# Performance work log

Hardware: AMD Instinct MI355X
Metric: run time of the kernel (lower is better)

The kernel has to match this reference:

```python
import jax, jax.numpy as jnp
import numpy as np

N_NODES = 50000
N_EDGES = 1200000
N_REL = 40
N_BASES = 30
EMB = 64
HID = 128
N_GRAPHS = 64


def rgcn_layer(h, src, dst, edge_type, comp, basis, root, bias):
    # W_r = sum_b comp[r,b] * basis[b]  -> [R, in, out]
    W = jnp.einsum('rb,bio->rio', comp, basis)
    n = h.shape[0]
    # aggregate source features per (target node, relation): mean aggregation (PyG RGCNConv default)
    seg = dst * N_REL + edge_type                      # [E]
    msgs = h[src]                                      # [E, in]  (gather)
    agg = jax.ops.segment_sum(msgs, seg, num_segments=n * N_REL)
    agg = agg.reshape(n, N_REL, -1)                    # [N, R, in]
    cnt = jax.ops.segment_sum(jnp.ones((src.shape[0],), h.dtype), seg,
                              num_segments=n * N_REL).reshape(n, N_REL, 1)
    agg = agg / jnp.maximum(cnt, 1.0)
    out = jnp.einsum('nri,rio->no', agg, W) + h @ root + bias
    return out


def setup_inputs() -> dict:
    key = jax.random.key(0)
    ks = jax.random.split(key, 12)
    x = jnp.arange(N_NODES, dtype=jnp.int64) if jax.config.jax_enable_x64 else jnp.arange(N_NODES, dtype=jnp.int32)
    edge_index = jax.random.randint(ks[0], (2, N_EDGES), 0, N_NODES)
    edge_type = jax.random.randint(ks[1], (N_EDGES,), 0, N_REL)
    batch = jnp.sort(jax.random.randint(ks[2], (N_NODES,), 0, N_GRAPHS))
    s = 0.05
    node_emb = jax.random.normal(ks[3], (N_NODES, EMB), jnp.float32)
    comp1 = jax.random.normal(ks[4], (N_REL, N_BASES), jnp.float32) * s
    basis1 = jax.random.normal(ks[5], (N_BASES, EMB, HID), jnp.float32) * s
    root1 = jax.random.normal(ks[6], (EMB, HID), jnp.float32) * s
    bias1 = jnp.zeros((HID,), jnp.float32)
    comp2 = jax.random.normal(ks[7], (N_REL, N_BASES), jnp.float32) * s
    basis2 = jax.random.normal(ks[8], (N_BASES, HID, HID), jnp.float32) * s
    root2 = jax.random.normal(ks[9], (HID, HID), jnp.float32) * s
    bias2 = jnp.zeros((HID,), jnp.float32)
    return {"x": x, "edge_index": edge_index, "edge_type": edge_type, "batch": batch,
            "node_emb": node_emb,
            "comp1": comp1, "basis1": basis1, "root1": root1, "bias1": bias1,
            "comp2": comp2, "basis2": basis2, "root2": root2, "bias2": bias2}


def reference(x, edge_index, edge_type, batch, node_emb,
              comp1, basis1, root1, bias1, comp2, basis2, root2, bias2):
    src, dst = edge_index[0], edge_index[1]
    h = node_emb[x]                                              # embedding lookup
    h = jax.nn.relu(rgcn_layer(h, src, dst, edge_type, comp1, basis1, root1, bias1))
    h = jax.nn.relu(rgcn_layer(h, src, dst, edge_type, comp2, basis2, root2, bias2))
    # global mean pool over graphs in batch
    sums = jax.ops.segment_sum(h, batch, num_segments=N_GRAPHS)  # [G, HID]
    cnts = jax.ops.segment_sum(jnp.ones((h.shape[0],), h.dtype), batch,
                               num_segments=N_GRAPHS)[:, None]
    return sums / jnp.maximum(cnts, 1.0)
```

## Files before the change

kernel.cpp:

```cpp
#include <hip/hip_runtime.h>


#define N_NODES 50000
#define N_EDGES 1200000
#define N_REL   40
#define N_BASES 30
#define EMB     64
#define HID     128
#define N_GRAPHS 64

#define NKEYC_MAX 160
#define PERM_CAP  ((size_t)N_EDGES + (size_t)NKEYC_MAX * 256)
#define SP_EPB    1024

typedef float f32x4  __attribute__((ext_vector_type(4)));
typedef short bf16x8 __attribute__((ext_vector_type(8)));

__device__ __forceinline__ unsigned short f2bf(float x) {
    unsigned int u = __float_as_uint(x);
    u = (u + 0x7FFFu + ((u >> 16) & 1u)) >> 16;
    return (unsigned short)u;
}
__device__ __forceinline__ float bflo(unsigned int u) { return __uint_as_float(u << 16); }
__device__ __forceinline__ float bfhi(unsigned int u) { return __uint_as_float(u & 0xffff0000u); }

#define OFF_WF1   ((size_t)0)
#define OFF_WF2   ((size_t)163840)
#define OFF_CNT   ((size_t)491520)
#define OFF_H1    ((size_t)2491520)
#define OFF_H2    ((size_t)8891520)
#define OFF_HB1   ((size_t)15291520)
#define OFF_HB2   ((size_t)16891520)
#define OFF_CNTG  ((size_t)20091520)
#define OFF_POOL  ((size_t)20091584)
#define OFF_PSRC  ((size_t)20099776)
#define OFF_POS   ((size_t)21340736)
#define OFF_PDST  ((size_t)22581696)
#define OFF_HCR   ((size_t)23822656)
#define OFF_CCR   ((size_t)23822816)
#define OFF_POCR  ((size_t)23822976)
#define OFF_HD    ((size_t)23823168)
#define OFF_CD    ((size_t)23873168)
#define OFF_POD   ((size_t)23923168)
#define OFF_RF1   ((size_t)23973184)
#define OFF_RF2   ((size_t)23977280)
#define OFF_PM    ((size_t)23985472)

template <int IN, int KT>
__global__ void k_Wfrag(const float* __restrict__ comp, const float* __restrict__ basis,
                        unsigned short* __restrict__ Wf) {
    const int FR = IN * HID;
    int idx = blockIdx.x * blockDim.x + threadIdx.x;
    if (idx >= N_REL * FR) return;
    int r = idx / FR, F = idx - r * FR;
    int j = F & 7, lane = (F >> 3) & 63, tt = F >> 9;
    int kt = tt % KT, ct = tt / KT;
    int k = kt * 32 + (lane >> 4) * 8 + j;
    int c = ct * 16 + (lane & 15);
    float s = 0.f;
#pragma unroll
    for (int b = 0; b < N_BASES; ++b)
        s += comp[r * N_BASES + b] * basis[((size_t)b * IN + k) * HID + c];
    Wf[idx] = f2bf(s);
}

template <int IN, int KT>
__global__ void k_rootfrag(const float* __restrict__ root, unsigned short* __restrict__ rf) {
    int idx = blockIdx.x * blockDim.x + threadIdx.x;
    if (idx >= IN * HID) return;
    int j = idx & 7, lane = (idx >> 3) & 63, tt = idx >> 9;
    int kt = tt % KT, ct = tt / KT;
    int k = kt * 32 + (lane >> 4) * 8 + j;
    int c = ct * 16 + (lane & 15);
    rf[idx] = f2bf(root[k * HID + c]);
}

__global__ void k_count(const int* __restrict__ dst, const int* __restrict__ etype,
                        float* __restrict__ cnt) {
    int e = blockIdx.x * blockDim.x + threadIdx.x;
    if (e >= N_EDGES) return;
    atomicAdd(&cnt[(size_t)dst[e] * N_REL + etype[e]], 1.0f);
}

__global__ void k_deg_inv(float* __restrict__ cnt, int* __restrict__ hist) {
    int n = blockIdx.x * blockDim.x + threadIdx.x;
    if (n >= N_NODES) return;
    float* row = cnt + (size_t)n * N_REL;
    float s = 0.f;
#pragma unroll 8
    for (int r = 0; r < N_REL; ++r) {
        float c = row[r];
        s += c;
        row[r] = 1.0f / fmaxf(c, 1.0f);
    }
    hist[n] = (int)(s + 0.5f);
}

__global__ void k_scan_d(const int* __restrict__ hist, int* __restrict__ po) {
    __shared__ int csum[256];
    int t = threadIdx.x;
    const int CH = (N_NODES + 255) / 256;
    int k0 = t * CH, k1 = min(k0 + CH, N_NODES);
    int s = 0;
    for (int k = k0; k < k1; ++k) s += hist[k];
    csum[t] = s;
    __syncthreads();
    if (t == 0) {
        int acc = 0;
        for (int i = 0; i < 256; ++i) { int v = csum[i]; csum[i] = acc; acc += v; }
        po[N_NODES] = acc;
    }
    __syncthreads();
    int base = csum[t];
    for (int k = k0; k < k1; ++k) { po[k] = base; base += hist[k]; }
}

__global__ void k_hist_cr(const int* __restrict__ dst, const int* __restrict__ etype,
                          int* __restrict__ hist, int chn, int nkeyc) {
    __shared__ int lh[NKEYC_MAX];
    int t = threadIdx.x;
    if (t < nkeyc) lh[t] = 0;
    __syncthreads();
    int e = blockIdx.x * blockDim.x + t;
    if (e < N_EDGES) atomicAdd(&lh[(dst[e] / chn) * N_REL + etype[e]], 1);
    __syncthreads();
    if (t < nkeyc && lh[t]) atomicAdd(&hist[t], lh[t]);
}

__global__ void k_scan_cr(const int* __restrict__ hist, int* __restrict__ po, int nkeyc) {
    if (threadIdx.x == 0) {
        int acc = 0;
        for (int k = 0; k < nkeyc; ++k) {
            po[k] = acc;
            acc += ((hist[k] + 255) >> 8) << 8;
        }
        po[nkeyc] = acc;
    }
}

__global__ void k_fill(int* __restrict__ ps_src, int* __restrict__ ps_os,
                       int* __restrict__ ps_dst, int dumprow) {
    for (size_t s = (size_t)blockIdx.x * blockDim.x + threadIdx.x; s < PERM_CAP;
         s += (size_t)gridDim.x * blockDim.x) {
        ps_src[s] = 0;
        ps_os[s] = dumprow;
        ps_dst[s] = 0;
    }
}

__global__ void k_scatter_s(const int* __restrict__ src, const int* __restrict__ dst,
                            const int* __restrict__ etype,
                            const int* __restrict__ po_cr, int* __restrict__ cur_cr,
                            const int* __restrict__ po_d, int* __restrict__ cur_d,
                            int* __restrict__ ps_src, int* __restrict__ ps_os,
                            int* __restrict__ ps_dst, int chn, int nkeyc) {
    __shared__ int lh[NKEYC_MAX], sbase[NKEYC_MAX];
    int t = threadIdx.x;
    if (t < nkeyc) lh[t] = 0;
    __syncthreads();
    int e0 = blockIdx.x * SP_EPB;
    int e_[4], key_[4];
#pragma unroll
    for (int i = 0; i < 4; ++i) {
        int e = e0 + t + i * 256;
        e_[i] = e;
        if (e < N_EDGES) {
            key_[i] = (dst[e] / chn) * N_REL + etype[e];
            atomicAdd(&lh[key_[i]], 1);
        }
    }
    __syncthreads();
    if (t < nkeyc) { if (lh[t]) sbase[t] = atomicAdd(&cur_cr[t], lh[t]); lh[t] = 0; }
    __syncthreads();
#pragma unroll
    for (int i = 0; i < 4; ++i) {
        if (e_[i] < N_EDGES) {
            int e = e_[i], key = key_[i];
            int d = dst[e];
            int p = atomicAdd(&lh[key], 1);
            int slot = po_cr[key] + sbase[key] + p;
            int os_g = po_d[d] + atomicAdd(&cur_d[d], 1);
            int os_l = os_g - po_d[(d / chn) * chn];
            ps_src[slot] = src[e];
            ps_os[slot] = os_l;
            ps_dst[slot] = d;
        }
    }
}

template <int IN, int KT>
__global__ __launch_bounds__(256, 4)
void k_rootgemm(const unsigned short* __restrict__ hb_in,
                const unsigned short* __restrict__ rf,
                const float* __restrict__ bias, float* __restrict__ h) {
    __shared__ unsigned short Wl[8 * KT * 64 * 8];
    {
        const f32x4* Wg = (const f32x4*)rf;
        f32x4* Wd = (f32x4*)Wl;
        for (int kk = threadIdx.x; kk < 8 * KT * 64; kk += 256) Wd[kk] = Wg[kk];
    }
    __syncthreads();

    int l = threadIdx.x & 63, wv = threadIdx.x >> 6;
    int lrow = l & 15, lk = l >> 4;
    int nbase = blockIdx.x * 64 + wv * 16;

    int nrow = min(nbase + lrow, N_NODES - 1);
    bf16x8 a[KT];
    const unsigned short* hrow = hb_in + (size_t)nrow * IN + lk * 8;
#pragma unroll
    for (int kt = 0; kt < KT; ++kt)
        a[kt] = *(const bf16x8*)(hrow + kt * 32);

    f32x4 acc[8];
#pragma unroll
    for (int ct = 0; ct < 8; ++ct) acc[ct] = (f32x4){0.f, 0.f, 0.f, 0.f};
#pragma unroll
    for (int ct = 0; ct < 8; ++ct) {
#pragma unroll
        for (int kt = 0; kt < KT; ++kt) {
            bf16x8 bb = *(const bf16x8*)(Wl + ((ct * KT + kt) * 64 + l) * 8);
            acc[ct] = __builtin_amdgcn_mfma_f32_16x16x32_bf16(a[kt], bb, acc[ct], 0, 0, 0);
        }
    }
#pragma unroll
    for (int q = 0; q < 4; ++q) {
        int n = nbase + lk * 4 + q;
        if (n < N_NODES) {
#pragma unroll
            for (int ct = 0; ct < 8; ++ct)
                h[(size_t)n * HID + ct * 16 + lrow] = acc[ct][q] + bias[ct * 16 + lrow];
        }
    }
}

template <int IN, int KT>
__global__ __launch_bounds__(256, 4)
void k_msg(const unsigned short* __restrict__ hb_in, const int* __restrict__ ps_src,
           const int* __restrict__ ps_os, const int* __restrict__ ps_dst,
           const float* __restrict__ invc,
           const int* __restrict__ po_cr,
           const unsigned short* __restrict__ Wf, unsigned int* __restrict__ pm) {
    __shared__ unsigned short Wl[8 * KT * 64 * 8];
    int slot0 = po_cr[0] + blockIdx.x * 256;
    if (slot0 >= po_cr[N_REL]) return;
    int r = 0;
    while (po_cr[r + 1] <= slot0) ++r;

    {
        const f32x4* Wg = (const f32x4*)(Wf + (size_t)r * (8 * KT * 64 * 8));
        f32x4* Wd = (f32x4*)Wl;
        for (int kk = threadIdx.x; kk < 8 * KT * 64; kk += 256) Wd[kk] = Wg[kk];
    }
    __syncthreads();

    int l = threadIdx.x & 63, wv = threadIdx.x >> 6;
    int lrow = l & 15, lk = l >> 4;

    for (int t = wv; t < 16; t += 4) {
        int slot = slot0 + t * 16 + lrow;
        int sv = ps_src[slot];
        int os = ps_os[slot];
        int d  = ps_dst[slot];
        float inv = invc[(size_t)d * N_REL + r];

        bf16x8 a[KT];
        const unsigned short* hrow = hb_in + (size_t)sv * IN + lk * 8;
#pragma unroll
        for (int kt = 0; kt < KT; ++kt)
            a[kt] = *(const bf16x8*)(hrow + kt * 32);

        f32x4 acc[8];
#pragma unroll
        for (int ct = 0; ct < 8; ++ct) acc[ct] = (f32x4){0.f, 0.f, 0.f, 0.f};
#pragma unroll
        for (int ct = 0; ct < 8; ++ct) {
#pragma unroll
            for (int kt = 0; kt < KT; ++kt) {
                bf16x8 bb = *(const bf16x8*)(Wl + ((ct * KT + kt) * 64 + l) * 8);
                acc[ct] = __builtin_amdgcn_mfma_f32_16x16x32_bf16(a[kt], bb, acc[ct], 0, 0, 0);
            }
        }
#pragma unroll
        for (int q = 0; q < 4; ++q) {
            int row = lk * 4 + q;
            int osq   = __shfl(os, row);
            float ivq = __shfl(inv, row);
            unsigned int* dp = pm + (size_t)osq * 64 + lrow;
#pragma unroll
            for (int cp = 0; cp < 4; ++cp) {
                unsigned int u = (unsigned int)f2bf(acc[2 * cp][q] * ivq)
                               | ((unsigned int)f2bf(acc[2 * cp + 1][q] * ivq) << 16);
                dp[cp * 16] = u;
            }
        }
    }
}

template <bool WRITE_HB>
__global__ __launch_bounds__(256, 8)
void k_reduce(const unsigned int* __restrict__ pm, const int* __restrict__ po_d,
              int n0chunk, int chn, float* __restrict__ h,
              unsigned short* __restrict__ hb_out) {
    int wv = threadIdx.x >> 6, p = threadIdx.x & 63;
    int n = n0chunk + blockIdx.x * 4 + wv;
    if (n >= n0chunk + chn) return;
    int pmbase = po_d[n0chunk];
    int b0 = po_d[n] - pmbase;
    int cn = po_d[n + 1] - pmbase - b0;
    float lo = 0.f, hi = 0.f;
    const unsigned int* rp = pm + (size_t)b0 * 64 + p;
    int k = 0;
    for (; k + 4 <= cn; k += 4) {
        unsigned int u0 = rp[0], u1 = rp[64], u2 = rp[128], u3 = rp[192];
        rp += 256;
        lo += bflo(u0) + bflo(u1) + bflo(u2) + bflo(u3);
        hi += bfhi(u0) + bfhi(u1) + bfhi(u2) + bfhi(u3);
    }
    for (; k < cn; ++k) {
        unsigned int u = rp[0];
        rp += 64;
        lo += bflo(u); hi += bfhi(u);
    }
    int cA = (p & 15) + 32 * (p >> 4);
    float* hp = h + (size_t)n * HID;
    float vA = fmaxf(hp[cA] + lo, 0.f);
    float vB = fmaxf(hp[cA + 16] + hi, 0.f);
    hp[cA] = vA;
    hp[cA + 16] = vB;
    if (WRITE_HB) {
        hb_out[(size_t)n * HID + cA] = f2bf(vA);
        hb_out[(size_t)n * HID + cA + 16] = f2bf(vB);
    }
}

__global__ void k_cvt_emb(const float* __restrict__ emb, const int* __restrict__ x,
                          unsigned short* __restrict__ hb) {
    int idx = blockIdx.x * blockDim.x + threadIdx.x;
    if (idx >= N_NODES * (EMB / 4)) return;
    int n = idx / (EMB / 4), c4 = idx % (EMB / 4);
    int row = x[n];
    float4 v = *(const float4*)(emb + (size_t)row * EMB + c4 * 4);
    ushort4 o = {f2bf(v.x), f2bf(v.y), f2bf(v.z), f2bf(v.w)};
    *(ushort4*)(hb + (size_t)n * EMB + c4 * 4) = o;
}

__global__ void k_gcount2(const int* __restrict__ batch, float* __restrict__ cntG) {
    int g = threadIdx.x;
    if (g >= N_GRAPHS) return;
    int lo = 0, hi = N_NODES;
    while (lo < hi) { int m = (lo + hi) >> 1; if (batch[m] < g) lo = m + 1; else hi = m; }
    int lb0 = lo;
    lo = 0; hi = N_NODES;
    while (lo < hi) { int m = (lo + hi) >> 1; if (batch[m] < g + 1) lo = m + 1; else hi = m; }
    cntG[g] = (float)(lo - lb0);
}

__global__ void k_pool(const float* __restrict__ h, const int* __restrict__ batch,
                       float* __restrict__ acc) {
    const int CH = 64;
    int n0 = blockIdx.x * CH;
    int o = threadIdx.x;
    int nend = min(n0 + CH, N_NODES);
    if (n0 >= N_NODES) return;
    int curg = batch[n0];
    float run = 0.f;
    for (int n = n0; n < nend; ++n) {
        int g = batch[n];
        if (g != curg) {
            atomicAdd(&acc[(size_t)curg * HID + o], run);
            run = 0.f;
            curg = g;
        }
        run += h[(size_t)n * HID + o];
    }
    atomicAdd(&acc[(size_t)curg * HID + o], run);
}

__global__ void k_final(const float* __restrict__ acc, const float* __restrict__ cntG,
                        float* __restrict__ out) {
    int idx = blockIdx.x * blockDim.x + threadIdx.x;
    if (idx >= N_GRAPHS * HID) return;
    int g = idx >> 7;
    out[idx] = acc[idx] / fmaxf(cntG[g], 1.0f);
}

extern "C" void kernel_launch(void* const* d_in, const int* in_sizes, int n_in,
                              void* d_out, int out_size, void* d_ws, size_t ws_size,
                              hipStream_t stream) {
    const int*   x         = (const int*)d_in[0];
    const int*   edge_index= (const int*)d_in[1];
    const int*   etype     = (const int*)d_in[2];
    const int*   batch     = (const int*)d_in[3];
    const float* node_emb  = (const float*)d_in[4];
    const float* comp1     = (const float*)d_in[5];
    const float* basis1    = (const float*)d_in[6];
    const float* root1     = (const float*)d_in[7];
    const float* bias1     = (const float*)d_in[8];
    const float* comp2     = (const float*)d_in[9];
    const float* basis2    = (const float*)d_in[10];
    const float* root2     = (const float*)d_in[11];
    const float* bias2     = (const float*)d_in[12];
    float* out = (float*)d_out;

    const int* src = edge_index;
    const int* dst = edge_index + N_EDGES;

    float* ws = (float*)d_ws;
    unsigned short* Wf1 = (unsigned short*)(ws + OFF_WF1);
    unsigned short* Wf2 = (unsigned short*)(ws + OFF_WF2);
    float* cnt  = ws + OFF_CNT;
    float* h1   = ws + OFF_H1;
    float* h2   = ws + OFF_H2;
    unsigned short* hb1 = (unsigned short*)(ws + OFF_HB1);
    unsigned short* hb2 = (unsigned short*)(ws + OFF_HB2);
    float* cntG = ws + OFF_CNTG;
    float* pool = ws + OFF_POOL;
    int*   ps_src = (int*)(ws + OFF_PSRC);
    int*   ps_os  = (int*)(ws + OFF_POS);
    int*   ps_dst = (int*)(ws + OFF_PDST);
    int*   hist_cr = (int*)(ws + OFF_HCR);
    int*   cur_cr  = (int*)(ws + OFF_CCR);
    int*   po_cr   = (int*)(ws + OFF_POCR);
    int*   hist_d  = (int*)(ws + OFF_HD);
    int*   cur_d   = (int*)(ws + OFF_CD);
    int*   po_d    = (int*)(ws + OFF_POD);
    unsigned short* rf1 = (unsigned short*)(ws + OFF_RF1);
    unsigned short* rf2 = (unsigned short*)(ws + OFF_RF2);
    unsigned int* pm = (unsigned int*)(ws + OFF_PM);

    size_t ws_floats = ws_size / sizeof(float);
    int nch = 4;
    if (ws_floats >= OFF_PM + ((size_t)N_EDGES / 1 + 12504) * 64) nch = 1;
    else if (ws_floats >= OFF_PM + ((size_t)N_EDGES / 2 + 12504) * 64) nch = 2;
    int chn = N_NODES / nch;
    int nkeyc = nch * N_REL;
    int capr = N_EDGES / nch + 12504;
    int gridm = (capr + 255) / 256 + N_REL;

    hipMemsetAsync(cnt, 0, (size_t)N_NODES * N_REL * sizeof(float), stream);
    hipMemsetAsync(cntG, 0, (size_t)(N_GRAPHS + N_GRAPHS * HID) * sizeof(float), stream);
    hipMemsetAsync(hist_cr, 0, 2 * NKEYC_MAX * sizeof(int), stream);
    hipMemsetAsync(cur_d, 0, N_NODES * sizeof(int), stream);

    k_count<<<(N_EDGES + 255) / 256, 256, 0, stream>>>(dst, etype, cnt);
    k_deg_inv<<<(N_NODES + 255) / 256, 256, 0, stream>>>(cnt, hist_d);
    k_scan_d<<<1, 256, 0, stream>>>(hist_d, po_d);
    k_hist_cr<<<(N_EDGES + 255) / 256, 256, 0, stream>>>(dst, etype, hist_cr, chn, nkeyc);
    k_scan_cr<<<1, 64, 0, stream>>>(hist_cr, po_cr, nkeyc);
    k_fill<<<2048, 256, 0, stream>>>(ps_src, ps_os, ps_dst, capr - 1);
    k_scatter_s<<<(N_EDGES + SP_EPB - 1) / SP_EPB, 256, 0, stream>>>(
        src, dst, etype, po_cr, cur_cr, po_d, cur_d, ps_src, ps_os, ps_dst, chn, nkeyc);

    k_Wfrag<EMB, 2><<<(N_REL * EMB * HID + 255) / 256, 256, 0, stream>>>(comp1, basis1, Wf1);
    k_Wfrag<HID, 4><<<(N_REL * HID * HID + 255) / 256, 256, 0, stream>>>(comp2, basis2, Wf2);
    k_rootfrag<EMB, 2><<<(EMB * HID + 255) / 256, 256, 0, stream>>>(root1, rf1);
    k_rootfrag<HID, 4><<<(HID * HID + 255) / 256, 256, 0, stream>>>(root2, rf2);

    k_cvt_emb<<<(N_NODES * (EMB / 4) + 255) / 256, 256, 0, stream>>>(node_emb, x, hb1);
    k_rootgemm<EMB, 2><<<(N_NODES + 63) / 64, 256, 0, stream>>>(hb1, rf1, bias1, h1);
    for (int c = 0; c < nch; ++c) {
        k_msg<EMB, 2><<<gridm, 256, 0, stream>>>(hb1, ps_src, ps_os, ps_dst, cnt,
                                                 po_cr + c * N_REL, Wf1, pm);
        k_reduce<true><<<chn / 4, 256, 0, stream>>>(pm, po_d, c * chn, chn, h1, hb2);
    }

    k_rootgemm<HID, 4><<<(N_NODES + 63) / 64, 256, 0, stream>>>(hb2, rf2, bias2, h2);
    for (int c = 0; c < nch; ++c) {
        k_msg<HID, 4><<<gridm, 256, 0, stream>>>(hb2, ps_src, ps_os, ps_dst, cnt,
                                                 po_cr + c * N_REL, Wf2, pm);
        k_reduce<false><<<chn / 4, 256, 0, stream>>>(pm, po_d, c * chn, chn, h2, nullptr);
    }

    k_gcount2<<<1, 64, 0, stream>>>(batch, cntG);
    k_pool<<<(N_NODES + 63) / 64, HID, 0, stream>>>(h2, batch, pool);
    k_final<<<(N_GRAPHS * HID + 255) / 256, 256, 0, stream>>>(pool, cntG, out);
}
```

Baseline: 1.031 ms.

## Sub-bucket edges by source range and transpose degree-inverse table

Each (dst-chunk, relation) edge bucket is further split by source-node slice, so the rows gathered within a bucket come from a narrower range of hb_in and should hit cache more often. The inverse-count table is transposed to relation-major so k_msg reads invc per relation contiguously by destination. A per-256-slot relation lookup table replaces the linear search over bucket offsets, and only the padding slots are filled instead of the whole permutation buffer. The cost is more buckets and therefore more padded slots and launched blocks, plus extra small setup kernels.

```diff
diff --git a/kernel.cpp b/kernel.cpp
--- a/kernel.cpp
+++ b/kernel.cpp
@@ -9,8 +9,8 @@
 #define HID     128
 #define N_GRAPHS 64
 
-#define NKEYC_MAX 160
-#define PERM_CAP  ((size_t)N_EDGES + (size_t)NKEYC_MAX * 256)
+#define NKEY      320
+#define PERM_CAP  ((size_t)N_EDGES + (size_t)NKEY * 256)
 #define SP_EPB    1024
 
 typedef float f32x4  __attribute__((ext_vector_type(4)));
@@ -34,17 +34,18 @@
 #define OFF_CNTG  ((size_t)20091520)
 #define OFF_POOL  ((size_t)20091584)
 #define OFF_PSRC  ((size_t)20099776)
-#define OFF_POS   ((size_t)21340736)
-#define OFF_PDST  ((size_t)22581696)
-#define OFF_HCR   ((size_t)23822656)
-#define OFF_CCR   ((size_t)23822816)
-#define OFF_POCR  ((size_t)23822976)
-#define OFF_HD    ((size_t)23823168)
-#define OFF_CD    ((size_t)23873168)
-#define OFF_POD   ((size_t)23923168)
-#define OFF_RF1   ((size_t)23973184)
-#define OFF_RF2   ((size_t)23977280)
-#define OFF_PM    ((size_t)23985472)
+#define OFF_POS   ((size_t)21381696)
+#define OFF_PDST  ((size_t)22663616)
+#define OFF_HCR   ((size_t)23945536)
+#define OFF_CCR   ((size_t)23945856)
+#define OFF_POCR  ((size_t)23946176)
+#define OFF_HD    ((size_t)23946560)
+#define OFF_CD    ((size_t)23996560)
+#define OFF_POD   ((size_t)24046560)
+#define OFF_RF1   ((size_t)24096576)
+#define OFF_RF2   ((size_t)24100672)
+#define OFF_BREL  ((size_t)24108864)
+#define OFF_PM    ((size_t)24110912)
 
 template <int IN, int KT>
 __global__ void k_Wfrag(const float* __restrict__ comp, const float* __restrict__ basis,
@@ -76,22 +77,21 @@
 }
 
 __global__ void k_count(const int* __restrict__ dst, const int* __restrict__ etype,
-                        float* __restrict__ cnt) {
+                        float* __restrict__ cnt_t) {
     int e = blockIdx.x * blockDim.x + threadIdx.x;
     if (e >= N_EDGES) return;
-    atomicAdd(&cnt[(size_t)dst[e] * N_REL + etype[e]], 1.0f);
-}
-
-__global__ void k_deg_inv(float* __restrict__ cnt, int* __restrict__ hist) {
+    atomicAdd(&cnt_t[(size_t)etype[e] * N_NODES + dst[e]], 1.0f);
+}
+
+__global__ void k_deg_inv(float* __restrict__ cnt_t, int* __restrict__ hist) {
     int n = blockIdx.x * blockDim.x + threadIdx.x;
     if (n >= N_NODES) return;
-    float* row = cnt + (size_t)n * N_REL;
     float s = 0.f;
 #pragma unroll 8
     for (int r = 0; r < N_REL; ++r) {
-        float c = row[r];
+        float c = cnt_t[(size_t)r * N_NODES + n];
         s += c;
-        row[r] = 1.0f / fmaxf(c, 1.0f);
+        cnt_t[(size_t)r * N_NODES + n] = 1.0f / fmaxf(c, 1.0f);
     }
     hist[n] = (int)(s + 0.5f);
 }
@@ -115,33 +115,47 @@
     for (int k = k0; k < k1; ++k) { po[k] = base; base += hist[k]; }
 }
 
-__global__ void k_hist_cr(const int* __restrict__ dst, const int* __restrict__ etype,
-                          int* __restrict__ hist, int chn, int nkeyc) {
-    __shared__ int lh[NKEYC_MAX];
-    int t = threadIdx.x;
-    if (t < nkeyc) lh[t] = 0;
-    __syncthreads();
-    int e = blockIdx.x * blockDim.x + t;
-    if (e < N_EDGES) atomicAdd(&lh[(dst[e] / chn) * N_REL + etype[e]], 1);
-    __syncthreads();
-    if (t < nkeyc && lh[t]) atomicAdd(&hist[t], lh[t]);
-}
-
-__global__ void k_scan_cr(const int* __restrict__ hist, int* __restrict__ po, int nkeyc) {
+__global__ void k_hist_cr(const int* __restrict__ src, const int* __restrict__ dst,
+                          const int* __restrict__ etype, int* __restrict__ hist,
+                          int chn, int slc, int sdiv) {
+    __shared__ int lh[NKEY];
+    for (int t = threadIdx.x; t < NKEY; t += 256) lh[t] = 0;
+    __syncthreads();
+    int e = blockIdx.x * blockDim.x + threadIdx.x;
+    if (e < N_EDGES) {
+        int key = (dst[e] / chn) * (N_REL * slc) + etype[e] * slc + src[e] / sdiv;
+        atomicAdd(&lh[key], 1);
+    }
+    __syncthreads();
+    for (int t = threadIdx.x; t < NKEY; t += 256)
+        if (lh[t]) atomicAdd(&hist[t], lh[t]);
+}
+
+__global__ void k_scan_cr(const int* __restrict__ hist, int* __restrict__ po) {
     if (threadIdx.x == 0) {
         int acc = 0;
-        for (int k = 0; k < nkeyc; ++k) {
+        for (int k = 0; k < NKEY; ++k) {
             po[k] = acc;
             acc += ((hist[k] + 255) >> 8) << 8;
         }
-        po[nkeyc] = acc;
-    }
-}
-
-__global__ void k_fill(int* __restrict__ ps_src, int* __restrict__ ps_os,
-                       int* __restrict__ ps_dst, int dumprow) {
-    for (size_t s = (size_t)blockIdx.x * blockDim.x + threadIdx.x; s < PERM_CAP;
-         s += (size_t)gridDim.x * blockDim.x) {
+        po[NKEY] = acc;
+    }
+}
+
+__global__ void k_brel(const int* __restrict__ po, unsigned char* __restrict__ brel,
+                       int slc) {
+    int k = blockIdx.x * blockDim.x + threadIdx.x;
+    if (k >= NKEY) return;
+    unsigned char r = (unsigned char)((k % (N_REL * slc)) / slc);
+    for (int b = po[k] >> 8; b < (po[k + 1] >> 8); ++b) brel[b] = r;
+}
+
+__global__ void k_fillpads(const int* __restrict__ hist, const int* __restrict__ po,
+                           int* __restrict__ ps_src, int* __restrict__ ps_os,
+                           int* __restrict__ ps_dst, int dumprow) {
+    int k = blockIdx.x;
+    int start = po[k] + hist[k], end = po[k + 1];
+    for (int s = start + threadIdx.x; s < end; s += blockDim.x) {
         ps_src[s] = 0;
         ps_os[s] = dumprow;
         ps_dst[s] = 0;
@@ -153,10 +167,10 @@
                             const int* __restrict__ po_cr, int* __restrict__ cur_cr,
                             const int* __restrict__ po_d, int* __restrict__ cur_d,
                             int* __restrict__ ps_src, int* __restrict__ ps_os,
-                            int* __restrict__ ps_dst, int chn, int nkeyc) {
-    __shared__ int lh[NKEYC_MAX], sbase[NKEYC_MAX];
+                            int* __restrict__ ps_dst, int chn, int slc, int sdiv) {
+    __shared__ int lh[NKEY], sbase[NKEY];
     int t = threadIdx.x;
-    if (t < nkeyc) lh[t] = 0;
+    for (int k = t; k < NKEY; k += 256) lh[k] = 0;
     __syncthreads();
     int e0 = blockIdx.x * SP_EPB;
     int e_[4], key_[4];
@@ -165,12 +179,15 @@
         int e = e0 + t + i * 256;
         e_[i] = e;
         if (e < N_EDGES) {
-            key_[i] = (dst[e] / chn) * N_REL + etype[e];
+            key_[i] = (dst[e] / chn) * (N_REL * slc) + etype[e] * slc + src[e] / sdiv;
             atomicAdd(&lh[key_[i]], 1);
         }
     }
     __syncthreads();
-    if (t < nkeyc) { if (lh[t]) sbase[t] = atomicAdd(&cur_cr[t], lh[t]); lh[t] = 0; }
+    for (int k = t; k < NKEY; k += 256) {
+        if (lh[k]) sbase[k] = atomicAdd(&cur_cr[k], lh[k]);
+        lh[k] = 0;
+    }
     __syncthreads();
 #pragma unroll
     for (int i = 0; i < 4; ++i) {
@@ -238,14 +255,13 @@
 __global__ __launch_bounds__(256, 4)
 void k_msg(const unsigned short* __restrict__ hb_in, const int* __restrict__ ps_src,
            const int* __restrict__ ps_os, const int* __restrict__ ps_dst,
-           const float* __restrict__ invc,
-           const int* __restrict__ po_cr,
+           const float* __restrict__ invc_t, const int* __restrict__ pob, int nbk,
+           const unsigned char* __restrict__ brel,
            const unsigned short* __restrict__ Wf, unsigned int* __restrict__ pm) {
     __shared__ unsigned short Wl[8 * KT * 64 * 8];
-    int slot0 = po_cr[0] + blockIdx.x * 256;
-    if (slot0 >= po_cr[N_REL]) return;
-    int r = 0;
-    while (po_cr[r + 1] <= slot0) ++r;
+    int slot0 = pob[0] + blockIdx.x * 256;
+    if (slot0 >= pob[nbk]) return;
+    int r = brel[slot0 >> 8];
 
     {
         const f32x4* Wg = (const f32x4*)(Wf + (size_t)r * (8 * KT * 64 * 8));
@@ -256,13 +272,14 @@
 
     int l = threadIdx.x & 63, wv = threadIdx.x >> 6;
     int lrow = l & 15, lk = l >> 4;
+    const float* invr = invc_t + (size_t)r * N_NODES;
 
     for (int t = wv; t < 16; t += 4) {
         int slot = slot0 + t * 16 + lrow;
         int sv = ps_src[slot];
         int os = ps_os[slot];
         int d  = ps_dst[slot];
-        float inv = invc[(size_t)d * N_REL + r];
+        float inv = invr[d];
 
         bf16x8 a[KT];
         const unsigned short* hrow = hb_in + (size_t)sv * IN + lk * 8;
@@ -409,7 +426,7 @@
     float* ws = (float*)d_ws;
     unsigned short* Wf1 = (unsigned short*)(ws + OFF_WF1);
     unsigned short* Wf2 = (unsigned short*)(ws + OFF_WF2);
-    float* cnt  = ws + OFF_CNT;
+    float* cnt_t = ws + OFF_CNT;
     float* h1   = ws + OFF_H1;
     float* h2   = ws + OFF_H2;
     unsigned short* hb1 = (unsigned short*)(ws + OFF_HB1);
@@ -427,6 +444,7 @@
     int*   po_d    = (int*)(ws + OFF_POD);
     unsigned short* rf1 = (unsigned short*)(ws + OFF_RF1);
     unsigned short* rf2 = (unsigned short*)(ws + OFF_RF2);
+    unsigned char* brel = (unsigned char*)(ws + OFF_BREL);
     unsigned int* pm = (unsigned int*)(ws + OFF_PM);
 
     size_t ws_floats = ws_size / sizeof(float);
@@ -434,23 +452,28 @@
     if (ws_floats >= OFF_PM + ((size_t)N_EDGES / 1 + 12504) * 64) nch = 1;
     else if (ws_floats >= OFF_PM + ((size_t)N_EDGES / 2 + 12504) * 64) nch = 2;
     int chn = N_NODES / nch;
-    int nkeyc = nch * N_REL;
+    int slc = 8 / nch;
+    int sdiv = 6250 * nch;
+    int nbk = NKEY / nch;
     int capr = N_EDGES / nch + 12504;
-    int gridm = (capr + 255) / 256 + N_REL;
-
-    hipMemsetAsync(cnt, 0, (size_t)N_NODES * N_REL * sizeof(float), stream);
+    int gridm = (capr + NKEY * 256 / nch) / 256 + 2;
+
+    hipMemsetAsync(cnt_t, 0, (size_t)N_NODES * N_REL * sizeof(float), stream);
     hipMemsetAsync(cntG, 0, (size_t)(N_GRAPHS + N_GRAPHS * HID) * sizeof(float), stream);
-    hipMemsetAsync(hist_cr, 0, 2 * NKEYC_MAX * sizeof(int), stream);
+    hipMemsetAsync(hist_cr, 0, 2 * NKEY * sizeof(int), stream);
     hipMemsetAsync(cur_d, 0, N_NODES * sizeof(int), stream);
 
-    k_count<<<(N_EDGES + 255) / 256, 256, 0, stream>>>(dst, etype, cnt);
-    k_deg_inv<<<(N_NODES + 255) / 256, 256, 0, stream>>>(cnt, hist_d);
+    k_count<<<(N_EDGES + 255) / 256, 256, 0, stream>>>(dst, etype, cnt_t);
+    k_deg_inv<<<(N_NODES + 255) / 256, 256, 0, stream>>>(cnt_t, hist_d);
     k_scan_d<<<1, 256, 0, stream>>>(hist_d, po_d);
-    k_hist_cr<<<(N_EDGES + 255) / 256, 256, 0, stream>>>(dst, etype, hist_cr, chn, nkeyc);
-    k_scan_cr<<<1, 64, 0, stream>>>(hist_cr, po_cr, nkeyc);
-    k_fill<<<2048, 256, 0, stream>>>(ps_src, ps_os, ps_dst, capr - 1);
+    k_hist_cr<<<(N_EDGES + 255) / 256, 256, 0, stream>>>(src, dst, etype, hist_cr,
+                                                         chn, slc, sdiv);
+    k_scan_cr<<<1, 64, 0, stream>>>(hist_cr, po_cr);
+    k_brel<<<2, 256, 0, stream>>>(po_cr, brel, slc);
+    k_fillpads<<<NKEY, 256, 0, stream>>>(hist_cr, po_cr, ps_src, ps_os, ps_dst, capr - 1);
     k_scatter_s<<<(N_EDGES + SP_EPB - 1) / SP_EPB, 256, 0, stream>>>(
-        src, dst, etype, po_cr, cur_cr, po_d, cur_d, ps_src, ps_os, ps_dst, chn, nkeyc);
+        src, dst, etype, po_cr, cur_cr, po_d, cur_d, ps_src, ps_os, ps_dst,
+        chn, slc, sdiv);
 
     k_Wfrag<EMB, 2><<<(N_REL * EMB * HID + 255) / 256, 256, 0, stream>>>(comp1, basis1, Wf1);
     k_Wfrag<HID, 4><<<(N_REL * HID * HID + 255) / 256, 256, 0, stream>>>(comp2, basis2, Wf2);
@@ -460,15 +483,15 @@
     k_cvt_emb<<<(N_NODES * (EMB / 4) + 255) / 256, 256, 0, stream>>>(node_emb, x, hb1);
     k_rootgemm<EMB, 2><<<(N_NODES + 63) / 64, 256, 0, stream>>>(hb1, rf1, bias1, h1);
     for (int c = 0; c < nch; ++c) {
-        k_msg<EMB, 2><<<gridm, 256, 0, stream>>>(hb1, ps_src, ps_os, ps_dst, cnt,
-                                                 po_cr + c * N_REL, Wf1, pm);
+        k_msg<EMB, 2><<<gridm, 256, 0, stream>>>(hb1, ps_src, ps_os, ps_dst, cnt_t,
+                                                 po_cr + c * nbk, nbk, brel, Wf1, pm);
         k_reduce<true><<<chn / 4, 256, 0, stream>>>(pm, po_d, c * chn, chn, h1, hb2);
     }
 
     k_rootgemm<HID, 4><<<(N_NODES + 63) / 64, 256, 0, stream>>>(hb2, rf2, bias2, h2);
     for (int c = 0; c < nch; ++c) {
-        k_msg<HID, 4><<<gridm, 256, 0, stream>>>(hb2, ps_src, ps_os, ps_dst, cnt,
-                                                 po_cr + c * N_REL, Wf2, pm);
+        k_msg<HID, 4><<<gridm, 256, 0, stream>>>(hb2, ps_src, ps_os, ps_dst, cnt_t,
+                                                 po_cr + c * nbk, nbk, brel, Wf2, pm);
         k_reduce<false><<<chn / 4, 256, 0, stream>>>(pm, po_d, c * chn, chn, h2, nullptr);
     }
 
```

Measured after the change: 1.068 ms. 1.04x slower.
